# Kernel tuning notes

Hardware: AMD Instinct MI355X
Metric: run time of the kernel (lower is better)

## Reference

```python
import jax, jax.numpy as jnp
import numpy as np
from jax import lax

B, L, D_MODEL = 4, 2048, 1024
EXPAND = 2
D_INNER = EXPAND * D_MODEL      # 2048
D_STATE = 32
D_CONV = 16
DT_RANK = (D_MODEL + 15) // 16  # 64 ('auto')
EPS = 1e-5


def setup_inputs() -> dict:
    key = jax.random.key(0)
    ks = jax.random.split(key, 10)
    s = 0.02
    x = jax.random.normal(ks[0], (B, L, D_MODEL), jnp.float32)
    norm_w = jnp.ones((D_MODEL,), jnp.float32)
    in_proj_w = jax.random.normal(ks[1], (2 * D_INNER, D_MODEL), jnp.float32) * s
    conv_w = jax.random.normal(ks[2], (D_INNER, D_CONV), jnp.float32) * (1.0 / np.sqrt(D_CONV))
    conv_b = jnp.zeros((D_INNER,), jnp.float32)
    x_proj_w = jax.random.normal(ks[3], (DT_RANK + 2 * D_STATE, D_INNER), jnp.float32) * s
    dt_proj_w = jax.random.normal(ks[4], (D_INNER, DT_RANK), jnp.float32) * (1.0 / np.sqrt(DT_RANK))
    # bias so softplus(dt_bias) ~ 1e-2, matching mamba dt init range
    dt_proj_b = jax.random.normal(ks[5], (D_INNER,), jnp.float32) * 0.1 - 4.6
    A_log = jnp.log(jnp.broadcast_to(jnp.arange(1, D_STATE + 1, dtype=jnp.float32), (D_INNER, D_STATE)))
    D_param = jnp.ones((D_INNER,), jnp.float32)
    out_proj_w = jax.random.normal(ks[6], (D_MODEL, D_INNER), jnp.float32) * s
    return dict(x=x, norm_w=norm_w, in_proj_w=in_proj_w, conv_w=conv_w, conv_b=conv_b,
                x_proj_w=x_proj_w, dt_proj_w=dt_proj_w, dt_proj_b=dt_proj_b,
                A_log=A_log, D_param=D_param, out_proj_w=out_proj_w)


def _rmsnorm(x, w):
    var = jnp.mean(x * x, axis=-1, keepdims=True)
    return x * lax.rsqrt(var + EPS) * w


def _silu(x):
    return x * jax.nn.sigmoid(x)


def _causal_depthwise_conv(x_bdl, w):
    # x_bdl: [B, D_INNER, L], w: [D_INNER, D_CONV] -> [B, D_INNER, L]
    rhs = w[:, None, :]  # [D_INNER, 1, D_CONV]
    return lax.conv_general_dilated(
        x_bdl, rhs, window_strides=(1,), padding=[(D_CONV - 1, 0)],
        dimension_numbers=('NCH', 'OIH', 'NCH'), feature_group_count=D_INNER)


def _mamba_forward(x, norm_w, in_proj_w, conv_w, conv_b, x_proj_w,
                   dt_proj_w, dt_proj_b, A_log, D_param, out_proj_w):
    xn = _rmsnorm(x, norm_w)                                  # [B,L,D]
    xz = jnp.einsum('bld,ed->ble', xn, in_proj_w)             # [B,L,2*D_INNER]
    xi, z = jnp.split(xz, 2, axis=-1)                          # each [B,L,D_INNER]
    xc = _causal_depthwise_conv(jnp.swapaxes(xi, 1, 2), conv_w)
    xc = _silu(jnp.swapaxes(xc, 1, 2) + conv_b)               # [B,L,D_INNER]
    x_dbl = jnp.einsum('bld,ed->ble', xc, x_proj_w)           # [B,L,R+2S]
    dt, Bm, Cm = jnp.split(x_dbl, [DT_RANK, DT_RANK + D_STATE], axis=-1)
    dt = jax.nn.softplus(jnp.einsum('blr,dr->bld', dt, dt_proj_w) + dt_proj_b)  # [B,L,D_INNER]
    A = -jnp.exp(A_log)                                        # [D_INNER, S]

    def step(h, inp):
        dt_t, x_t, B_t, C_t = inp  # [B,D_INNER],[B,D_INNER],[B,S],[B,S]
        dA = jnp.exp(dt_t[..., None] * A)                     # [B,D_INNER,S]
        h = dA * h + (dt_t * x_t)[..., None] * B_t[:, None, :]
        y = jnp.einsum('bds,bs->bd', h, C_t)
        return h, y

    h0 = jnp.zeros((B, D_INNER, D_STATE), xc.dtype)
    seq = (jnp.swapaxes(dt, 0, 1), jnp.swapaxes(xc, 0, 1),
           jnp.swapaxes(Bm, 0, 1), jnp.swapaxes(Cm, 0, 1))
    _, ys = lax.scan(step, h0, seq)                            # [L,B,D_INNER]
    y = jnp.swapaxes(ys, 0, 1) + D_param * xc                  # skip term
    y = y * _silu(z)                                           # gate
    out = jnp.einsum('bld,ed->ble', y, out_proj_w)             # [B,L,D]
    return out + x                                             # residual


def reference(x, norm_w, in_proj_w, conv_w, conv_b, x_proj_w, dt_proj_w,
              dt_proj_b, A_log, D_param, out_proj_w):
    return _mamba_forward(x, norm_w, in_proj_w, conv_w, conv_b, x_proj_w,
                          dt_proj_w, dt_proj_b, A_log, D_param, out_proj_w)
```

## Files before the change

kernel.cpp:

```cpp
#include <hip/hip_runtime.h>
#include <hip/hip_bf16.h>
#include <type_traits>

typedef float v4f __attribute__((ext_vector_type(4)));
typedef short v8s __attribute__((ext_vector_type(8)));
typedef __hip_bfloat16 bf16;

#define B_SZ 4
#define L_SZ 2048
#define DMODEL 1024
#define DINNER 2048
#define DSTATE 32
#define DCONV 16
#define DTRANK 64
#define MROWS (B_SZ * L_SZ)
#define GCHUNK 32
#define CHUNK 64

__global__ __launch_bounds__(256) void cvt_bf16_kernel(
    const float* __restrict__ in, bf16* __restrict__ out, int n) {
  int i = blockIdx.x * 256 + threadIdx.x;
  if (i < n) out[i] = __float2bfloat16(in[i]);
}

__global__ __launch_bounds__(256) void rmsnorm_kernel(
    const float* __restrict__ x, const float* __restrict__ w, bf16* __restrict__ xn) {
  const int row = blockIdx.x;
  const int tid = threadIdx.x;
  const float* xr = x + (size_t)row * DMODEL;
  float vals[4];
  float ss = 0.f;
#pragma unroll
  for (int i = 0; i < 4; ++i) {
    float v = xr[tid + i * 256];
    vals[i] = v;
    ss += v * v;
  }
#pragma unroll
  for (int o = 32; o > 0; o >>= 1) ss += __shfl_down(ss, o, 64);
  __shared__ float wsum[4];
  if ((tid & 63) == 0) wsum[tid >> 6] = ss;
  __syncthreads();
  float tot = wsum[0] + wsum[1] + wsum[2] + wsum[3];
  float scale = rsqrtf(tot / (float)DMODEL + 1e-5f);
#pragma unroll
  for (int i = 0; i < 4; ++i) {
    float wv = w[tid + i * 256];
    xn[(size_t)row * DMODEL + tid + i * 256] = __float2bfloat16(vals[i] * scale * wv);
  }
}

template <typename OutT, bool ADD_RES, bool SPLIT, bool KSPLIT>
__global__ __launch_bounds__(256) void gemm_nt(
    const bf16* __restrict__ A, const bf16* __restrict__ Bw,
    OutT* __restrict__ C, OutT* __restrict__ C2,
    const float* __restrict__ resid, int M, int N, int kLen, int lda, int nsplit) {
  constexpr int BM = 128, BN = 128, BK = 32;
  __shared__ __align__(16) short As[BM * BK];
  __shared__ __align__(16) short Bs[BN * BK];
  const int m0 = blockIdx.x * BM;
  const int n0 = blockIdx.y * BN;
  const int kOff = KSPLIT ? blockIdx.z * kLen : 0;
  const int tid = threadIdx.x;
  const int wave = tid >> 6;
  const int lane = tid & 63;
  const int wm = (wave >> 1) * 64;
  const int wn = (wave & 1) * 64;
  const int lrow = lane & 15;
  const int kgrp = lane >> 4;

  v4f acc[4][4] = {};

  for (int k0 = 0; k0 < kLen; k0 += BK) {
    __syncthreads();
#pragma unroll
    for (int p = 0; p < 2; ++p) {
      const int ebase = p * 2048 + wave * 512;
      const int e = ebase + lane * 8;
      const int r = e >> 5, c = e & 31;
      __builtin_amdgcn_global_load_lds(
          (const __attribute__((address_space(1))) unsigned int*)(A + (size_t)(m0 + r) * lda + kOff + k0 + c),
          (__attribute__((address_space(3))) unsigned int*)&As[ebase], 16, 0, 0);
      __builtin_amdgcn_global_load_lds(
          (const __attribute__((address_space(1))) unsigned int*)(Bw + (size_t)(n0 + r) * lda + kOff + k0 + c),
          (__attribute__((address_space(3))) unsigned int*)&Bs[ebase], 16, 0, 0);
    }
    __syncthreads();

    v8s af[4], bfr[4];
#pragma unroll
    for (int i = 0; i < 4; ++i)
      af[i] = *(const v8s*)&As[(wm + i * 16 + lrow) * BK + kgrp * 8];
#pragma unroll
    for (int j = 0; j < 4; ++j)
      bfr[j] = *(const v8s*)&Bs[(wn + j * 16 + lrow) * BK + kgrp * 8];
#pragma unroll
    for (int i = 0; i < 4; ++i)
#pragma unroll
      for (int j = 0; j < 4; ++j)
        acc[i][j] = __builtin_amdgcn_mfma_f32_16x16x32_bf16(af[i], bfr[j], acc[i][j], 0, 0, 0);
  }

  OutT* Cw = C;
  if (KSPLIT) Cw += (size_t)blockIdx.z * M * N;
  int gcb = n0;
  int ldc = N;
  if (SPLIT) {
    ldc = nsplit;
    if (n0 >= nsplit) { Cw = C2; gcb = n0 - nsplit; }
  }
  const int crow = (lane >> 4) * 4;
  const int ccol = lane & 15;
#pragma unroll
  for (int i = 0; i < 4; ++i) {
#pragma unroll
    for (int j = 0; j < 4; ++j) {
      int gr = m0 + wm + i * 16 + crow;
      int gc = gcb + wn + j * 16 + ccol;
#pragma unroll
      for (int r = 0; r < 4; ++r) {
        float v = acc[i][j][r];
        size_t off = (size_t)(gr + r) * ldc + gc;
        if (ADD_RES) v += resid[off];
        if constexpr (std::is_same<OutT, float>::value)
          Cw[off] = v;
        else
          Cw[off] = __float2bfloat16(v);
      }
    }
  }
}

#define SBAR()  asm volatile("s_barrier" ::: "memory")
#define LGKM0() asm volatile("s_waitcnt lgkmcnt(0)" ::: "memory")

#define LOAD_A(BUF, MH) \
  { _Pragma("unroll") for (int m_ = 0; m_ < 4; ++m_) { \
      _Pragma("unroll") for (int kk_ = 0; kk_ < 2; ++kk_) { \
        const int row_ = wvm + (MH) * 64 + m_ * 16 + lrow; \
        const int slot_ = (kk_ * 4 + kgrp) ^ (lrow & 7); \
        af[m_ * 2 + kk_] = *(const v8s*)&Als[BUF][row_ * 64 + slot_ * 8]; } } }

#define LOAD_B(BUF, NH) \
  { _Pragma("unroll") for (int n_ = 0; n_ < 2; ++n_) { \
      _Pragma("unroll") for (int kk_ = 0; kk_ < 2; ++kk_) { \
        const int row_ = wvn + (NH) * 32 + n_ * 16 + lrow; \
        const int slot_ = (kk_ * 4 + kgrp) ^ (lrow & 7); \
        bfr[n_ * 2 + kk_] = *(const v8s*)&Bls[BUF][row_ * 64 + slot_ * 8]; } } }

#define MFMA_Q(MH, NH) \
  { __builtin_amdgcn_s_setprio(1); \
    _Pragma("unroll") for (int m_ = 0; m_ < 4; ++m_) \
    _Pragma("unroll") for (int n_ = 0; n_ < 2; ++n_) \
    _Pragma("unroll") for (int kk_ = 0; kk_ < 2; ++kk_) \
      acc[(MH) * 4 + m_][(NH) * 2 + n_] = __builtin_amdgcn_mfma_f32_16x16x32_bf16( \
          af[m_ * 2 + kk_], bfr[n_ * 2 + kk_], acc[(MH) * 4 + m_][(NH) * 2 + n_], 0, 0, 0); \
    __builtin_amdgcn_s_setprio(0); }

template <typename OutT, bool ADD_RES, bool SPLIT>
__global__ __launch_bounds__(512) void gemm256_nt(
    const bf16* __restrict__ A, const bf16* __restrict__ Bw,
    OutT* __restrict__ C, OutT* __restrict__ C2,
    const float* __restrict__ resid, int M, int N, int K, int lda, int nsplit) {
  __shared__ __align__(16) short Als[2][256 * 64];
  __shared__ __align__(16) short Bls[2][256 * 64];

  const int nbx = gridDim.x;
  const int nwg = nbx * gridDim.y;
  const int orig = blockIdx.y * nbx + blockIdx.x;
  const int cpx = nwg >> 3;
  const int swz = (orig & 7) * cpx + (orig >> 3);
  const int m0 = (swz % nbx) * 256;
  const int n0 = (swz / nbx) * 256;

  const int tid = threadIdx.x;
  const int wave = tid >> 6;
  const int lane = tid & 63;
  const int lrow = lane & 15;
  const int kgrp = lane >> 4;
  const int wvm = (wave >> 2) * 128;
  const int wvn = (wave & 3) * 64;

  const int NT = K >> 6;

  const int rl_ = wave * 8 + (lane >> 3);
  const int csrc_ = (((lane & 7) ^ (lane >> 3)) << 3);
  auto stage = [&](int h) {
    const int th = h >> 2;
    if (th >= NT) return;
    const int hh = h & 3;
    const int bufb = th & 1;
    const bf16* src = (hh < 2) ? A : Bw;
    const int row0 = ((hh < 2) ? m0 : n0) + (hh & 1) * 128;
    short* dst = ((hh < 2) ? &Als[0][0] + bufb * (256 * 64)
                           : &Bls[0][0] + bufb * (256 * 64)) + (hh & 1) * (128 * 64);
    const int k0 = th * 64;
#pragma unroll
    for (int j = 0; j < 2; ++j) {
      __builtin_amdgcn_global_load_lds(
          (const __attribute__((address_space(1))) unsigned int*)
              (src + (size_t)(row0 + j * 64 + rl_) * lda + k0 + csrc_),
          (__attribute__((address_space(3))) unsigned int*)
              (dst + j * 4096 + wave * 512),
          16, 0, 0);
    }
  };

  v8s af[8], bfr[4];
  v4f acc[8][4] = {};

  stage(0); stage(1); stage(2); stage(3); stage(4); stage(5);
  asm volatile("s_waitcnt vmcnt(4)" ::: "memory");
  SBAR();

  for (int t = 0; t < NT; t += 2) {
    const int hb = t * 4 + 6;
    const bool last = (t + 2 >= NT);
    LOAD_A(0, 0); LOAD_B(0, 0);
    stage(hb + 0);
    SBAR(); LGKM0();
    MFMA_Q(0, 0);
    SBAR();
    LOAD_B(0, 1);
    stage(hb + 1);
    SBAR(); LGKM0();
    MFMA_Q(0, 1);
    SBAR();
    LOAD_A(0, 1);
    stage(hb + 2);
    SBAR(); LGKM0();
    MFMA_Q(1, 1);
    SBAR();
    LOAD_B(0, 0);
    stage(hb + 3);
    if (last) { asm volatile("s_waitcnt vmcnt(0)" ::: "memory"); }
    else      { asm volatile("s_waitcnt vmcnt(4)" ::: "memory"); }
    SBAR(); LGKM0();
    MFMA_Q(1, 0);
    SBAR();
    LOAD_A(1, 0); LOAD_B(1, 0);
    stage(hb + 4);
    SBAR(); LGKM0();
    MFMA_Q(0, 0);
    SBAR();
    LOAD_B(1, 1);
    stage(hb + 5);
    SBAR(); LGKM0();
    MFMA_Q(0, 1);
    SBAR();
    LOAD_A(1, 1);
    stage(hb + 6);
    SBAR(); LGKM0();
    MFMA_Q(1, 1);
    SBAR();
    LOAD_B(1, 0);
    stage(hb + 7);
    if (!last) { asm volatile("s_waitcnt vmcnt(4)" ::: "memory"); }
    SBAR(); LGKM0();
    MFMA_Q(1, 0);
    SBAR();
  }

  OutT* Cw = C;
  int gcb = n0;
  int ldc = N;
  if (SPLIT) {
    ldc = nsplit;
    if (n0 >= nsplit) { Cw = C2; gcb = n0 - nsplit; }
  }
  const int crow = kgrp * 4;
  const int ccol = lrow;
#pragma unroll
  for (int mf = 0; mf < 8; ++mf) {
#pragma unroll
    for (int nf = 0; nf < 4; ++nf) {
      const int gr = m0 + wvm + mf * 16 + crow;
      const int gc = gcb + wvn + nf * 16 + ccol;
#pragma unroll
      for (int r = 0; r < 4; ++r) {
        float v = acc[mf][nf][r];
        size_t off = (size_t)(gr + r) * ldc + gc;
        if (ADD_RES) v += resid[off];
        if constexpr (std::is_same<OutT, float>::value)
          Cw[off] = v;
        else
          Cw[off] = __float2bfloat16(v);
      }
    }
  }
}

__global__ __launch_bounds__(256) void reduce4_kernel(
    const float* __restrict__ part, float* __restrict__ out, int n) {
  int i = blockIdx.x * 256 + threadIdx.x;
  if (i < n)
    out[i] = part[i] + part[i + n] + part[i + 2 * n] + part[i + 3 * n];
}

__global__ __launch_bounds__(256) void conv_kernel(
    const bf16* __restrict__ xi, const float* __restrict__ cw,
    const float* __restrict__ cb, bf16* __restrict__ xc) {
  const int l0 = blockIdx.x * 64;
  const int d0 = blockIdx.y * 64;
  const int b = blockIdx.z;
  __shared__ float xs[79][64];
  __shared__ float wsm[16][64];
  __shared__ float cbs[64];
  const int tid = threadIdx.x;
  for (int e = tid; e < 79 * 64; e += 256) {
    int r = e >> 6, d = e & 63;
    int lt = l0 - 15 + r;
    float v = 0.f;
    if (lt >= 0)
      v = __bfloat162float(xi[((size_t)b * L_SZ + lt) * DINNER + d0 + d]);
    xs[r][d] = v;
  }
  for (int e = tid; e < 16 * 64; e += 256) {
    int j = e >> 6, d = e & 63;
    wsm[j][d] = cw[(size_t)(d0 + d) * DCONV + j];
  }
  if (tid < 64) cbs[tid] = cb[d0 + tid];
  __syncthreads();
  const int d = tid & 63;
  const int lb = tid >> 6;
  for (int li = lb; li < 64; li += 4) {
    float a = 0.f;
#pragma unroll
    for (int j = 0; j < DCONV; ++j) a += xs[li + j][d] * wsm[j][d];
    a += cbs[d];
    float s = a / (1.f + __expf(-a));
    xc[((size_t)b * L_SZ + l0 + li) * DINNER + d0 + d] = __float2bfloat16(s);
  }
}

__global__ __launch_bounds__(256) void dtproj_kernel(
    const float* __restrict__ xdbl, const float* __restrict__ W,
    const float* __restrict__ bias, bf16* __restrict__ dtr) {
  const int d = blockIdx.x * 256 + threadIdx.x;
  const int r0 = blockIdx.y * 32;
  float wreg[64];
#pragma unroll
  for (int j = 0; j < 64; ++j)
    wreg[j] = W[(size_t)d * DTRANK + j];
  const float bia = bias[d];
  const float* __restrict__ xbase = xdbl + (size_t)r0 * 128;
#pragma unroll 2
  for (int r = 0; r < 32; ++r) {
    const float* __restrict__ xr = xbase + (size_t)r * 128;
    float acc = bia;
#pragma unroll
    for (int j = 0; j < 64; ++j) acc += xr[j] * wreg[j];
    float dt = (acc > 20.f) ? acc : log1pf(__expf(acc));
    dtr[(size_t)(r0 + r) * DINNER + d] = __float2bfloat16(dt);
  }
}

template <bool PHASE1>
__global__ __launch_bounds__(256) void scan_chunk_kernel(
    const float* __restrict__ xdbl, const bf16* __restrict__ dtr,
    const bf16* __restrict__ xc, const bf16* __restrict__ z,
    const float* __restrict__ A_log, const float* __restrict__ D_param,
    const float* __restrict__ hbuf_in, float* __restrict__ hbuf_out,
    float* __restrict__ dtsum, bf16* __restrict__ yg) {
  const int b    = blockIdx.x >> 8;
  const int g    = (blockIdx.x >> 3) & 31;
  const int dgrp = blockIdx.x & 7;
  const int tid  = threadIdx.x;
  const int d    = dgrp * 256 + tid;

  const float A0 = -__expf(A_log[(size_t)d * DSTATE]);
  float h[DSTATE];
  if constexpr (PHASE1) {
#pragma unroll
    for (int s = 0; s < DSTATE; ++s) h[s] = 0.f;
  } else {
    const float* hp = hbuf_in + (((size_t)(b * GCHUNK + g) << 16) + ((size_t)d << 5));
#pragma unroll
    for (int q = 0; q < 8; ++q) {
      v4f hv = *(const v4f*)&hp[q * 4];
      h[q * 4] = hv[0]; h[q * 4 + 1] = hv[1]; h[q * 4 + 2] = hv[2]; h[q * 4 + 3] = hv[3];
    }
  }
  const float Dv = D_param[d];
  float dtacc = 0.f;

  const size_t rowbase = (size_t)b * L_SZ + g * CHUNK;
  const float* __restrict__ bcbase = xdbl + rowbase * 128 + 64;

  const bf16* dtp = dtr + rowbase * DINNER + d;
  const bf16* xcp = xc  + rowbase * DINNER + d;
  const bf16* zp  = z   + rowbase * DINNER + d;
  bf16* ygp = yg + rowbase * DINNER + d;

#pragma unroll 2
  for (int i = 0; i < CHUNK; ++i) {
    const float* __restrict__ bc = bcbase + (size_t)i * 128;
    float dt = __bfloat162float(dtp[(size_t)i * DINNER]);
    float xv = __bfloat162float(xcp[(size_t)i * DINNER]);
    float dtx = dt * xv;
    float w  = __expf(-dt);
    float eq = __expf(dt * A0);
    float w2 = w * w;
    float w3 = w2 * w;
    float w4 = w2 * w2;
    if constexpr (PHASE1) dtacc += dt;
    float y = 0.f;
#pragma unroll
    for (int q = 0; q < 8; ++q) {
      float e0 = eq, e1 = eq * w, e2 = eq * w2, e3 = eq * w3;
      h[q * 4 + 0] = e0 * h[q * 4 + 0] + dtx * bc[q * 4 + 0];
      h[q * 4 + 1] = e1 * h[q * 4 + 1] + dtx * bc[q * 4 + 1];
      h[q * 4 + 2] = e2 * h[q * 4 + 2] + dtx * bc[q * 4 + 2];
      h[q * 4 + 3] = e3 * h[q * 4 + 3] + dtx * bc[q * 4 + 3];
      if constexpr (!PHASE1) {
        y += h[q * 4 + 0] * bc[32 + q * 4 + 0];
        y += h[q * 4 + 1] * bc[32 + q * 4 + 1];
        y += h[q * 4 + 2] * bc[32 + q * 4 + 2];
        y += h[q * 4 + 3] * bc[32 + q * 4 + 3];
      }
      eq *= w4;
    }
    if constexpr (!PHASE1) {
      float zf = __bfloat162float(zp[(size_t)i * DINNER]);
      float yv = y + Dv * xv;
      float gt = zf / (1.f + __expf(-zf));
      ygp[(size_t)i * DINNER] = __float2bfloat16(yv * gt);
    }
  }

  if constexpr (PHASE1) {
    float* hop = hbuf_out + (((size_t)(b * GCHUNK + g) << 16) + ((size_t)d << 5));
#pragma unroll
    for (int q = 0; q < 8; ++q) {
      v4f hv;
      hv[0] = h[q * 4]; hv[1] = h[q * 4 + 1]; hv[2] = h[q * 4 + 2]; hv[3] = h[q * 4 + 3];
      *(v4f*)&hop[q * 4] = hv;
    }
    dtsum[(size_t)(b * GCHUNK + g) * DINNER + d] = dtacc;
  }
}

__global__ __launch_bounds__(256) void scan_combine_kernel(
    const float* __restrict__ A_log, const float* __restrict__ dtsum,
    float* __restrict__ hbuf) {
  const int gid = blockIdx.x * 256 + threadIdx.x;
  const int b = gid >> 16;
  const int ds = gid & 65535;
  const int dd = ds >> 5;
  const float As = -__expf(A_log[ds]);
  float hs = 0.f;
  for (int g = 0; g < GCHUNK; ++g) {
    size_t idx = ((size_t)(b * GCHUNK + g) << 16) + ds;
    float hl = hbuf[idx];
    hbuf[idx] = hs;
    float W = __expf(As * dtsum[(size_t)(b * GCHUNK + g) * DINNER + dd]);
    hs = W * hs + hl;
  }
}

extern "C" void kernel_launch(void* const* d_in, const int* in_sizes, int n_in,
                              void* d_out, int out_size, void* d_ws, size_t ws_size,
                              hipStream_t stream) {
  const float* x         = (const float*)d_in[0];
  const float* norm_w    = (const float*)d_in[1];
  const float* in_proj_w = (const float*)d_in[2];
  const float* conv_w    = (const float*)d_in[3];
  const float* conv_b    = (const float*)d_in[4];
  const float* x_proj_w  = (const float*)d_in[5];
  const float* dt_proj_w = (const float*)d_in[6];
  const float* dt_proj_b = (const float*)d_in[7];
  const float* A_log     = (const float*)d_in[8];
  const float* D_param   = (const float*)d_in[9];
  const float* out_proj_w= (const float*)d_in[10];
  float* out = (float*)d_out;

  char* w = (char*)d_ws;
  bf16* bufA  = (bf16*)w; w += (size_t)MROWS * DINNER * 2;
  bf16* bufB  = (bf16*)w; w += (size_t)MROWS * DINNER * 2;
  bf16* xcb   = (bf16*)w; w += (size_t)MROWS * DINNER * 2;
  float* xdbl = (float*)w; w += (size_t)MROWS * 128 * 4;
  bf16* w_out = (bf16*)w; w += (size_t)DMODEL * DINNER * 2;
  float* dtsm = (float*)w; w += (size_t)B_SZ * GCHUNK * DINNER * 4;

  char* o = (char*)d_out;
  bf16* xn   = (bf16*)o; o += (size_t)MROWS * DMODEL * 2;
  bf16* w_in = (bf16*)o; o += (size_t)(2 * DINNER) * DMODEL * 2;
  bf16* w_xp = (bf16*)o;
  float* hbuf = (float*)d_out;
  float* xpart = (float*)bufA;

  cvt_bf16_kernel<<<(2 * DINNER * DMODEL + 255) / 256, 256, 0, stream>>>(
      in_proj_w, w_in, 2 * DINNER * DMODEL);
  cvt_bf16_kernel<<<(128 * DINNER + 255) / 256, 256, 0, stream>>>(
      x_proj_w, w_xp, 128 * DINNER);
  cvt_bf16_kernel<<<(DMODEL * DINNER + 255) / 256, 256, 0, stream>>>(
      out_proj_w, w_out, DMODEL * DINNER);

  rmsnorm_kernel<<<MROWS, 256, 0, stream>>>(x, norm_w, xn);

  gemm256_nt<bf16, false, true><<<dim3(MROWS / 256, (2 * DINNER) / 256), 512, 0, stream>>>(
      xn, w_in, bufA, bufB, nullptr, MROWS, 2 * DINNER, DMODEL, DMODEL, DINNER);

  conv_kernel<<<dim3(L_SZ / 64, DINNER / 64, B_SZ), 256, 0, stream>>>(
      bufA, conv_w, conv_b, xcb);

  gemm_nt<float, false, false, true><<<dim3(MROWS / 128, 1, 4), 256, 0, stream>>>(
      xcb, w_xp, xpart, nullptr, nullptr, MROWS, 128, DINNER / 4, DINNER, 0);
  reduce4_kernel<<<(MROWS * 128) / 256, 256, 0, stream>>>(xpart, xdbl, MROWS * 128);

  dtproj_kernel<<<dim3(DINNER / 256, MROWS / 32), 256, 0, stream>>>(
      xdbl, dt_proj_w, dt_proj_b, bufA);

  scan_chunk_kernel<true><<<B_SZ * GCHUNK * (DINNER / 256), 256, 0, stream>>>(
      xdbl, bufA, xcb, bufB, A_log, D_param, nullptr, hbuf, dtsm, nullptr);
  scan_combine_kernel<<<(B_SZ * DINNER * DSTATE) / 256, 256, 0, stream>>>(
      A_log, dtsm, hbuf);
  scan_chunk_kernel<false><<<B_SZ * GCHUNK * (DINNER / 256), 256, 0, stream>>>(
      xdbl, bufA, xcb, bufB, A_log, D_param, hbuf, nullptr, nullptr, bufB);

  gemm256_nt<float, true, false><<<dim3(MROWS / 256, DMODEL / 256), 512, 0, stream>>>(
      bufB, w_out, out, nullptr, x, MROWS, DMODEL, DINNER, DINNER, 0);
}
```

Before: 570.5 us.

## Double-buffer B fragments, regroup tile swizzle, use 128-tile GEMM for out_proj

The 256x256 GEMM now keeps two B-fragment register sets, so the repeated LDS reload of the first B half is skipped. Its workgroup swizzle is reworked to group eight M tiles per N column for better L2 reuse. The out_proj GEMM switches from the 256-tile kernel to the 128-tile gemm_nt, which gives 512 workgroups instead of 128 to fill the CUs better. The cost is more registers in the big kernel and less per-block data reuse in out_proj.

```diff
diff --git a/kernel.cpp b/kernel.cpp
--- a/kernel.cpp
+++ b/kernel.cpp
@@ -141,20 +141,20 @@
         const int slot_ = (kk_ * 4 + kgrp) ^ (lrow & 7); \
         af[m_ * 2 + kk_] = *(const v8s*)&Als[BUF][row_ * 64 + slot_ * 8]; } } }
 
-#define LOAD_B(BUF, NH) \
+#define LOAD_B(BUF, NH, DST) \
   { _Pragma("unroll") for (int n_ = 0; n_ < 2; ++n_) { \
       _Pragma("unroll") for (int kk_ = 0; kk_ < 2; ++kk_) { \
         const int row_ = wvn + (NH) * 32 + n_ * 16 + lrow; \
         const int slot_ = (kk_ * 4 + kgrp) ^ (lrow & 7); \
-        bfr[n_ * 2 + kk_] = *(const v8s*)&Bls[BUF][row_ * 64 + slot_ * 8]; } } }
-
-#define MFMA_Q(MH, NH) \
+        DST[n_ * 2 + kk_] = *(const v8s*)&Bls[BUF][row_ * 64 + slot_ * 8]; } } }
+
+#define MFMA_Q(MH, NH, BFA) \
   { __builtin_amdgcn_s_setprio(1); \
     _Pragma("unroll") for (int m_ = 0; m_ < 4; ++m_) \
     _Pragma("unroll") for (int n_ = 0; n_ < 2; ++n_) \
     _Pragma("unroll") for (int kk_ = 0; kk_ < 2; ++kk_) \
       acc[(MH) * 4 + m_][(NH) * 2 + n_] = __builtin_amdgcn_mfma_f32_16x16x32_bf16( \
-          af[m_ * 2 + kk_], bfr[n_ * 2 + kk_], acc[(MH) * 4 + m_][(NH) * 2 + n_], 0, 0, 0); \
+          af[m_ * 2 + kk_], BFA[n_ * 2 + kk_], acc[(MH) * 4 + m_][(NH) * 2 + n_], 0, 0, 0); \
     __builtin_amdgcn_s_setprio(0); }
 
 template <typename OutT, bool ADD_RES, bool SPLIT>
@@ -166,12 +166,16 @@
   __shared__ __align__(16) short Bls[2][256 * 64];
 
   const int nbx = gridDim.x;
-  const int nwg = nbx * gridDim.y;
+  const int nby = gridDim.y;
+  const int nwg = nbx * nby;
   const int orig = blockIdx.y * nbx + blockIdx.x;
-  const int cpx = nwg >> 3;
-  const int swz = (orig & 7) * cpx + (orig >> 3);
-  const int m0 = (swz % nbx) * 256;
-  const int n0 = (swz / nbx) * 256;
+  const int idx = (orig & 7) * (nwg >> 3) + (orig >> 3);
+  const int g   = idx / (8 * nby);
+  const int rem = idx - g * (8 * nby);
+  const int nt  = rem >> 3;
+  const int mi  = rem & 7;
+  const int m0 = (g * 8 + mi) * 256;
+  const int n0 = nt * 256;
 
   const int tid = threadIdx.x;
   const int wave = tid >> 6;
@@ -206,7 +210,7 @@
     }
   };
 
-  v8s af[8], bfr[4];
+  v8s af[8], bfrE[4], bfrO[4];
   v4f acc[8][4] = {};
 
   stage(0); stage(1); stage(2); stage(3); stage(4); stage(5);
@@ -216,48 +220,46 @@
   for (int t = 0; t < NT; t += 2) {
     const int hb = t * 4 + 6;
     const bool last = (t + 2 >= NT);
-    LOAD_A(0, 0); LOAD_B(0, 0);
+    LOAD_A(0, 0); LOAD_B(0, 0, bfrE);
     stage(hb + 0);
     SBAR(); LGKM0();
-    MFMA_Q(0, 0);
-    SBAR();
-    LOAD_B(0, 1);
+    MFMA_Q(0, 0, bfrE);
+    SBAR();
+    LOAD_B(0, 1, bfrO);
     stage(hb + 1);
     SBAR(); LGKM0();
-    MFMA_Q(0, 1);
+    MFMA_Q(0, 1, bfrO);
     SBAR();
     LOAD_A(0, 1);
     stage(hb + 2);
     SBAR(); LGKM0();
-    MFMA_Q(1, 1);
-    SBAR();
-    LOAD_B(0, 0);
+    MFMA_Q(1, 1, bfrO);
+    SBAR();
     stage(hb + 3);
     if (last) { asm volatile("s_waitcnt vmcnt(0)" ::: "memory"); }
     else      { asm volatile("s_waitcnt vmcnt(4)" ::: "memory"); }
     SBAR(); LGKM0();
-    MFMA_Q(1, 0);
-    SBAR();
-    LOAD_A(1, 0); LOAD_B(1, 0);
+    MFMA_Q(1, 0, bfrE);
+    SBAR();
+    LOAD_A(1, 0); LOAD_B(1, 0, bfrE);
     stage(hb + 4);
     SBAR(); LGKM0();
-    MFMA_Q(0, 0);
-    SBAR();
-    LOAD_B(1, 1);
+    MFMA_Q(0, 0, bfrE);
+    SBAR();
+    LOAD_B(1, 1, bfrO);
     stage(hb + 5);
     SBAR(); LGKM0();
-    MFMA_Q(0, 1);
+    MFMA_Q(0, 1, bfrO);
     SBAR();
     LOAD_A(1, 1);
     stage(hb + 6);
     SBAR(); LGKM0();
-    MFMA_Q(1, 1);
-    SBAR();
-    LOAD_B(1, 0);
+    MFMA_Q(1, 1, bfrO);
+    SBAR();
     stage(hb + 7);
     if (!last) { asm volatile("s_waitcnt vmcnt(4)" ::: "memory"); }
     SBAR(); LGKM0();
-    MFMA_Q(1, 0);
+    MFMA_Q(1, 0, bfrE);
     SBAR();
   }
 
@@ -518,6 +520,6 @@
   scan_chunk_kernel<false><<<B_SZ * GCHUNK * (DINNER / 256), 256, 0, stream>>>(
       xdbl, bufA, xcb, bufB, A_log, D_param, hbuf, nullptr, nullptr, bufB);
 
-  gemm256_nt<float, true, false><<<dim3(MROWS / 256, DMODEL / 256), 512, 0, stream>>>(
+  gemm_nt<float, true, false, false><<<dim3(MROWS / 128, DMODEL / 128), 256, 0, stream>>>(
       bufB, w_out, out, nullptr, x, MROWS, DMODEL, DINNER, DINNER, 0);
 }
```

New measurement: 568.8 us. About the same (-0.3%).
